# Kernel tuning notes

Hardware: AMD Instinct MI355X
Metric: run time of the kernel (lower is better)

The kernel has to match this reference:

```python
import jax, jax.numpy as jnp
import numpy as np

NC = 5  # num_clusters == unfold window size


def conv1x3(x, w, b):
    # x: (B, Cin, H, W); w: (Cout, Cin, 1, 3); padding (0,1) like torch Conv2d
    y = jax.lax.conv_general_dilated(
        x, w, window_strides=(1, 1), padding=((0, 0), (1, 1)),
        dimension_numbers=("NCHW", "OIHW", "NCHW"))
    return y + b[None, :, None, None]


def setup_inputs() -> dict:
    key = jax.random.key(0)
    ks = jax.random.split(key, 8)
    b, h, l, d = 8, 8, 1024, 64
    dm = h * d  # d_model = 512
    f32 = jnp.float32
    s_conv1 = 1.0 / np.sqrt(dm * 3)
    s_conv2 = 1.0 / np.sqrt(NC * 3)
    s_lin = 1.0 / np.sqrt(NC)
    return {
        "Q": jax.random.normal(ks[0], (b, h, l, d), f32),
        "K": jax.random.normal(ks[1], (b, h, l, d), f32),
        "V": jax.random.normal(ks[2], (b, h, l, d), f32),
        "w_proj_k": jax.random.normal(ks[3], (NC, dm, 1, 3), f32) * s_conv1,
        "b_proj_k": jnp.zeros((NC,), f32),
        "w_proj_back": jax.random.normal(ks[4], (dm, NC, 1, 3), f32) * s_conv2,
        "b_proj_back": jnp.zeros((dm,), f32),
        "w_ck": jax.random.normal(ks[5], (NC, NC), f32) * s_lin,
        "b_ck": jnp.zeros((NC,), f32),
        "w_cq": jax.random.normal(ks[6], (NC, NC), f32) * s_lin,
        "b_cq": jnp.zeros((NC,), f32),
    }


def reference(Q, K, V, w_proj_k, b_proj_k, w_proj_back, b_proj_back,
              w_ck, b_ck, w_cq, b_cq):
    b, h, l, d = Q.shape
    u = NC  # unfolding window
    # --- padded unfold along batch dim: window i is K_padded[i:i+u] ---
    K_padded = jnp.concatenate(
        [jnp.zeros((u, h, l, d), Q.dtype), K[1:]], axis=0)  # (u+b-1, h, l, d)
    idx = jnp.arange(b)[:, None] + jnp.arange(u)[None, :]     # (b, u)
    Kw = K_padded[idx]                                        # (b, u, h, l, d)
    Kw = jnp.transpose(Kw, (0, 2, 3, 4, 1))                   # (b, h, l, d, u) == torch unfold layout
    K_unfold = Kw.reshape(b, h * d, l, u)                     # raw reshape, matches torch
    # --- project to clusters ---
    ckp = jax.nn.relu(conv1x3(K_unfold, w_proj_k, b_proj_k))  # (b, NC, l, u)
    ckp = jnp.transpose(ckp, (0, 2, 3, 1))                    # (b, l, u, NC)
    cluster_k = jax.nn.softmax(ckp @ w_ck.T + b_ck, axis=-1)
    cluster_q = jax.nn.softmax(ckp @ w_cq.T + b_cq, axis=-1)
    # --- distributional loss ---
    mu = jnp.mean(cluster_q, axis=-1)                         # (b, l, u)
    sigma = jax.nn.softplus(jnp.std(cluster_q, axis=-1, ddof=1))  # unbiased std like torch
    x = jnp.mean(cluster_k, axis=-1)
    log_prob = -0.5 * ((x - mu) / sigma) ** 2 - jnp.log(sigma) - 0.5 * jnp.log(2 * jnp.pi)
    # CrossEntropyLoss(mu, mu): class dim is axis=1 (l); soft-label targets = mu
    ce = -jnp.mean(jnp.sum(mu * jax.nn.log_softmax(mu, axis=1), axis=1))
    loss = -jnp.mean(log_prob) + ce
    # --- masked triangular cluster attention ---
    scores = jnp.einsum('blpc,bluc->blpu', cluster_q, cluster_k) / u  # (b, l, u, u)
    mask = jnp.triu(jnp.ones((u, u), bool), k=1)
    scores = jnp.where(mask, -1e9, scores)
    attn = jax.nn.softmax(scores, axis=-1)
    cluster_q2 = jnp.einsum('blpu,bluc->blpc', attn, cluster_q)       # (b, l, u, NC)
    # --- project back & second attention ---
    cc = jax.nn.relu(conv1x3(jnp.transpose(cluster_q2, (0, 3, 1, 2)),
                             w_proj_back, b_proj_back))               # (b, h*d, l, u)
    cluster_center = cc.reshape(b, h, u, l, d)                        # raw reshape, matches torch
    scores_center = jnp.einsum('bhqd,bhckd->bhqk', Q, cluster_center) # sums over c and d
    attn2 = jax.nn.softmax(scores_center, axis=-1)
    context = jnp.einsum('bhqk,bhkd->bhqd', attn2, V)
    return (context, loss)
```

## Files before the change

kernel.cpp:

```cpp
#include <hip/hip_runtime.h>
#include <math.h>

#define L 1024
#define D 64
#define H 8
#define B 8

#define WS_G     0
#define WS_MU    107520
#define WS_Q2T   148480
#define WS_Q2T_BYTE   593920u
#define WS_DSC_BYTE   1740800u
#define WS_KHI_BYTE   1740816u
#define WS_KLO_BYTE   10129424u
#define WS_VTHI_BYTE  18518032u
#define WS_VTLO_BYTE  26906640u
#define WS_V_END      35295248u

typedef __attribute__((ext_vector_type(8))) short bf16x8;
typedef __attribute__((ext_vector_type(4))) float f32x4;

__device__ __forceinline__ ushort f2bf(float x) {
  unsigned b = __builtin_bit_cast(unsigned, x);
  return (ushort)((b + 0x7FFFu + ((b >> 16) & 1u)) >> 16);
}
__device__ __forceinline__ float bf2f(ushort u) {
  unsigned t = ((unsigned)u) << 16;
  return __builtin_bit_cast(float, t);
}

__global__ __launch_bounds__(256) void k_part(const float* __restrict__ K,
                                              const float* __restrict__ wpk,
                                              float* __restrict__ G) {
  const int tid = threadIdx.x, lane = tid & 63, wid = tid >> 6;
  const int lq = blockIdx.x;
  const int bip = blockIdx.y + 1;
  __shared__ float w_s[512 * 16];
  __shared__ float red[3][64][16];
  for (int i = tid; i < 512 * 16; i += 256) {
    int c = i >> 4, f = i & 15;
    w_s[i] = (f < 15) ? wpk[((f / 3) * 512 + c) * 3 + (f % 3)] : 0.f;
  }
  __syncthreads();
  float acc[15];
#pragma unroll
  for (int f = 0; f < 15; ++f) acc[f] = 0.f;
  const float* Kb = K + (size_t)bip * (H * L * D);
  const int c0 = wid * 128;
#pragma unroll 4
  for (int c = c0; c < c0 + 128; ++c) {
    float val = Kb[((c >> 6) * L + ((c & 63) << 4) + lq) * D + lane];
    const float4* wr = (const float4*)&w_s[c * 16];
    float4 w0 = wr[0], w1 = wr[1], w2 = wr[2], w3 = wr[3];
    acc[0] = fmaf(val, w0.x, acc[0]);  acc[1] = fmaf(val, w0.y, acc[1]);
    acc[2] = fmaf(val, w0.z, acc[2]);  acc[3] = fmaf(val, w0.w, acc[3]);
    acc[4] = fmaf(val, w1.x, acc[4]);  acc[5] = fmaf(val, w1.y, acc[5]);
    acc[6] = fmaf(val, w1.z, acc[6]);  acc[7] = fmaf(val, w1.w, acc[7]);
    acc[8] = fmaf(val, w2.x, acc[8]);  acc[9] = fmaf(val, w2.y, acc[9]);
    acc[10] = fmaf(val, w2.z, acc[10]); acc[11] = fmaf(val, w2.w, acc[11]);
    acc[12] = fmaf(val, w3.x, acc[12]); acc[13] = fmaf(val, w3.y, acc[13]);
    acc[14] = fmaf(val, w3.z, acc[14]);
  }
  if (wid) {
#pragma unroll
    for (int f = 0; f < 15; ++f) red[wid - 1][lane][f] = acc[f];
  }
  __syncthreads();
  if (wid == 0) {
#pragma unroll
    for (int f = 0; f < 15; ++f)
      acc[f] += red[0][lane][f] + red[1][lane][f] + red[2][lane][f];
    float* dst = G + ((size_t)blockIdx.y * 1024 + (lq << 6) + lane) * 15;
#pragma unroll
    for (int f = 0; f < 15; ++f) dst[f] = acc[f];
  }
}

__global__ __launch_bounds__(256) void k_chain(const float* __restrict__ G,
    const float* __restrict__ b_pk, const float* __restrict__ w_ck,
    const float* __restrict__ b_ck, const float* __restrict__ w_cq,
    const float* __restrict__ b_cq, float* __restrict__ mu_out,
    float* __restrict__ q2t, double* __restrict__ dsc) {
  int g = blockIdx.x * 256 + threadIdx.x;
  int bi = g >> 10, li = g & 1023;
  float ckp[5][5];
#pragma unroll
  for (int j = 0; j < 5; ++j) {
#pragma unroll
    for (int nc = 0; nc < 5; ++nc) {
      float s = b_pk[nc];
#pragma unroll
      for (int t = 0; t < 3; ++t) {
        int w = j + t - 1;
        int bip = bi + w - 4;
        if (w >= 0 && w < 5 && bip >= 1)
          s += G[(size_t)((bip - 1) * 1024 + li) * 15 + nc * 3 + t];
      }
      ckp[j][nc] = fmaxf(s, 0.f);
    }
  }
  float cq[5][5], ck[5][5];
  float lp_sum = 0.f;
#pragma unroll
  for (int j = 0; j < 5; ++j) {
    float vk[5], vq[5];
#pragma unroll
    for (int m = 0; m < 5; ++m) {
      float sk = b_ck[m], sq = b_cq[m];
#pragma unroll
      for (int n = 0; n < 5; ++n) {
        sk = fmaf(ckp[j][n], w_ck[m * 5 + n], sk);
        sq = fmaf(ckp[j][n], w_cq[m * 5 + n], sq);
      }
      vk[m] = sk; vq[m] = sq;
    }
    float mk = vk[0], mq = vq[0];
#pragma unroll
    for (int m = 1; m < 5; ++m) { mk = fmaxf(mk, vk[m]); mq = fmaxf(mq, vq[m]); }
    float sk = 0.f, sq = 0.f;
#pragma unroll
    for (int m = 0; m < 5; ++m) {
      vk[m] = expf(vk[m] - mk); sk += vk[m];
      vq[m] = expf(vq[m] - mq); sq += vq[m];
    }
    float rk = 1.f / sk, rq = 1.f / sq;
    float mu = 0.f, x = 0.f;
#pragma unroll
    for (int m = 0; m < 5; ++m) {
      ck[j][m] = vk[m] * rk; cq[j][m] = vq[m] * rq;
      mu += cq[j][m]; x += ck[j][m];
    }
    mu *= 0.2f; x *= 0.2f;
    float var = 0.f;
#pragma unroll
    for (int m = 0; m < 5; ++m) { float d0 = cq[j][m] - mu; var += d0 * d0; }
    var *= 0.25f;
    float sg = log1pf(expf(sqrtf(var)));
    float z = (x - mu) / sg;
    lp_sum += -0.5f * z * z - logf(sg) - 0.91893853320467274f;
    mu_out[(size_t)g * 5 + j] = mu;
  }
  float* q2p = q2t + (((size_t)bi * 35) << 10) + li;
#pragma unroll
  for (int pp = 0; pp < 5; ++pp) {
    float sc[5]; float mx = -3.0e38f;
    for (int u2 = 0; u2 <= pp; ++u2) {
      float d0 = 0.f;
#pragma unroll
      for (int c = 0; c < 5; ++c) d0 = fmaf(cq[pp][c], ck[u2][c], d0);
      sc[u2] = d0 * 0.2f;
      mx = fmaxf(mx, sc[u2]);
    }
    float den = 0.f;
    for (int u2 = 0; u2 <= pp; ++u2) { sc[u2] = expf(sc[u2] - mx); den += sc[u2]; }
    float rd = 1.f / den;
    float q2v[5] = {0.f, 0.f, 0.f, 0.f, 0.f};
    for (int u2 = 0; u2 <= pp; ++u2) {
      float a = sc[u2] * rd;
#pragma unroll
      for (int c = 0; c < 5; ++c) q2v[c] = fmaf(a, cq[u2][c], q2v[c]);
    }
#pragma unroll
    for (int c = 0; c < 5; ++c) q2p[(size_t)(((pp + 1) * 5 + c)) << 10] = q2v[c];
  }
  for (int off = 1; off < 64; off <<= 1) lp_sum += __shfl_xor(lp_sum, off, 64);
  __shared__ float wsum[4];
  int tid = threadIdx.x;
  if ((tid & 63) == 0) wsum[tid >> 6] = lp_sum;
  __syncthreads();
  if (tid == 0) atomicAdd(dsc, (double)(wsum[0] + wsum[1] + wsum[2] + wsum[3]));
}

__global__ __launch_bounds__(256) void k_ce(const float* __restrict__ mu,
                                            double* __restrict__ dsc) {
  int bi = blockIdx.x / 5, u = blockIdx.x % 5;
  int tid = threadIdx.x;
  const float* base = mu + (size_t)bi * L * 5 + u;
  float v[4];
#pragma unroll
  for (int k = 0; k < 4; ++k) v[k] = base[(tid + 256 * k) * 5];
  float mx = fmaxf(fmaxf(v[0], v[1]), fmaxf(v[2], v[3]));
  for (int off = 1; off < 64; off <<= 1) mx = fmaxf(mx, __shfl_xor(mx, off, 64));
  __shared__ float sh[4];
  if ((tid & 63) == 0) sh[tid >> 6] = mx;
  __syncthreads();
  mx = fmaxf(fmaxf(sh[0], sh[1]), fmaxf(sh[2], sh[3]));
  __syncthreads();
  float se = 0.f;
#pragma unroll
  for (int k = 0; k < 4; ++k) se += expf(v[k] - mx);
  for (int off = 1; off < 64; off <<= 1) se += __shfl_xor(se, off, 64);
  if ((tid & 63) == 0) sh[tid >> 6] = se;
  __syncthreads();
  float lse = mx + logf(sh[0] + sh[1] + sh[2] + sh[3]);
  __syncthreads();
  float part = 0.f;
#pragma unroll
  for (int k = 0; k < 4; ++k) part += v[k] * (v[k] - lse);
  for (int off = 1; off < 64; off <<= 1) part += __shfl_xor(part, off, 64);
  if ((tid & 63) == 0) sh[tid >> 6] = part;
  __syncthreads();
  if (tid == 0) atomicAdd(dsc + 1, (double)(sh[0] + sh[1] + sh[2] + sh[3]));
}

__global__ __launch_bounds__(256) void k_cback(const float* __restrict__ q2t,
    const float* __restrict__ wb, const float* __restrict__ bb,
    float* __restrict__ keff) {
  __shared__ float ls[1280];
  const int id = blockIdx.x;
  const int bi = id >> 11, cog = (id >> 4) & 127, lt = id & 15;
  const int tid = threadIdx.x, w = tid >> 6, lane = tid & 63;
  const int co = cog * 4 + w;
  const int li2 = (lt << 6) + lane;
  const float* xb = q2t + (((size_t)bi * 35) << 10) + li2;
  float xt[35];
#pragma unroll
  for (int k = 0; k < 35; ++k) xt[k] = xb[(size_t)k << 10];
  float wbl[15];
#pragma unroll
  for (int t = 0; t < 3; ++t)
#pragma unroll
    for (int c = 0; c < 5; ++c) wbl[t * 5 + c] = wb[co * 15 + c * 3 + t];
  const float bias = bb[co];
#pragma unroll
  for (int j = 0; j < 5; ++j) {
    float s = bias;
#pragma unroll
    for (int i = 0; i < 15; ++i) s = fmaf(xt[j * 5 + i], wbl[i], s);
    ls[w * 320 + lane * 5 + j] = fmaxf(s, 0.f);
  }
  __syncthreads();
  const int base_lo = (cog * 4) * 5120 + (lt << 6) * 5;
#pragma unroll
  for (int k = 0; k < 5; ++k) {
    int e = tid + (k << 8);
    float val = ls[e];
    int we = (int)((unsigned)e / 320u);
    int off = e - we * 320;
    int flat = base_lo + we * 5120 + off;
    int q = flat >> 16;
    int hh = (q * 205) >> 10;
    int idx = (((bi << 3) + hh) << 16) + (flat & 65535);
    atomicAdd(&keff[idx], val);
  }
}

__global__ __launch_bounds__(256) void k_kfold(const float* __restrict__ keff,
    ushort* __restrict__ Khi_g, ushort* __restrict__ Klo_g) {
  int g = blockIdx.x * 256 + threadIdx.x;
  float sum = keff[g];
  int li = (g >> 6) & 1023, dd = g & 63;
  int bh = g >> 16;
  int kt = li >> 6, key = li & 63, c = dd >> 2, e = dd & 3;
  int idx = ((bh * 16 + kt) << 12) + (key << 6) + ((c ^ (key & 15)) << 2) + e;
  ushort hb = f2bf(sum);
  Khi_g[idx] = hb;
  Klo_g[idx] = f2bf(sum - bf2f(hb));
}

__global__ __launch_bounds__(256) void k_vprep(const float* __restrict__ V,
    ushort* __restrict__ Vthi_g, ushort* __restrict__ Vtlo_g) {
  __shared__ float t[64][65];
  const int tile = blockIdx.x;
  const float* Vb = V + ((size_t)tile << 12);
  const int tid = threadIdx.x;
  {
    int key = tid >> 2, c0 = (tid & 3) << 4;
#pragma unroll
    for (int i = 0; i < 4; ++i) {
      float4 v = *(const float4*)(Vb + key * 64 + c0 + 4 * i);
      t[key][c0 + 4 * i + 0] = v.x; t[key][c0 + 4 * i + 1] = v.y;
      t[key][c0 + 4 * i + 2] = v.z; t[key][c0 + 4 * i + 3] = v.w;
    }
  }
  __syncthreads();
  int d = tid >> 2, q4 = tid & 3;
#pragma unroll
  for (int q = 0; q < 4; ++q) {
    int kc = q4 * 4 + q;
    ushort hv[4], lv[4];
#pragma unroll
    for (int e = 0; e < 4; ++e) {
      float x = t[kc * 4 + e][d];
      ushort hb = f2bf(x);
      hv[e] = hb;
      lv[e] = f2bf(x - bf2f(hb));
    }
    int idx = (tile << 12) + (d << 6) + ((kc ^ (d & 15)) << 2);
    ushort4 h4; h4.x = hv[0]; h4.y = hv[1]; h4.z = hv[2]; h4.w = hv[3];
    ushort4 l4; l4.x = lv[0]; l4.y = lv[1]; l4.z = lv[2]; l4.w = lv[3];
    *(ushort4*)(&Vthi_g[idx]) = h4;
    *(ushort4*)(&Vtlo_g[idx]) = l4;
  }
}

template<bool VPREP>
__global__ __launch_bounds__(256) void k_attn(const float* __restrict__ Q,
    const ushort* __restrict__ Khi_g, const ushort* __restrict__ Klo_g,
    const ushort* __restrict__ Vthi_g, const ushort* __restrict__ Vtlo_g,
    const float* __restrict__ V, float* __restrict__ Out) {
  __shared__ ushort smem[2][16384];
  const int tid = threadIdx.x;
  const int lane = tid & 63;
  const int w = tid >> 6;
  const int lq = lane & 15;
  const int g = lane >> 4;
  const int id = blockIdx.x;
  const int bh = ((id & 7) << 3) + (id >> 6);
  const int qb = (id >> 3) & 7;
  const int q0 = qb << 7;
  const float* Qb = Q + ((size_t)bh * L + q0 + w * 32) * D;
  const float* Vb = V + (size_t)bh * L * D;
  const int tb = bh * 16;

  int cx0 = ((g) ^ lq) << 2, cx1 = ((g + 4) ^ lq) << 2;
  int cx2 = ((g + 8) ^ lq) << 2, cx3 = ((g + 12) ^ lq) << 2;

  bf16x8 qh[2][2], qlo[2][2];
#pragma unroll
  for (int qs = 0; qs < 2; ++qs) {
    const float* Qr = Qb + (qs * 16 + lq) * D;
#pragma unroll
    for (int ds = 0; ds < 2; ++ds) {
      float4 x0 = *(const float4*)(Qr + 4 * g + 32 * ds);
      float4 x1 = *(const float4*)(Qr + 4 * g + 16 + 32 * ds);
      float xs[8] = {x0.x, x0.y, x0.z, x0.w, x1.x, x1.y, x1.z, x1.w};
      bf16x8 h, l;
#pragma unroll
      for (int j = 0; j < 8; ++j) {
        ushort hb = f2bf(xs[j]);
        h[j] = (short)hb;
        l[j] = (short)f2bf(xs[j] - bf2f(hb));
      }
      qh[qs][ds] = h; qlo[qs][ds] = l;
    }
  }

  const ushort* warr;
  int wdst;
  if (VPREP) {
    warr = (w == 0) ? Khi_g : (w == 1) ? Klo_g : (w == 2) ? Vthi_g : Vtlo_g;
    wdst = w << 12;
  } else {
    warr = ((w < 2) ? Khi_g : Klo_g);
    wdst = ((w >> 1) << 12) + ((w & 1) << 11);
  }

#define STAGE(buf_, kt_) do {                                                  \
    const ushort* src_ = warr + ((size_t)(tb + (kt_)) << 12) +                 \
                         (VPREP ? 0 : ((w & 1) << 11)) + lane * 8;             \
    ushort* dst_ = &smem[buf_][wdst];                                          \
    _Pragma("unroll")                                                          \
    for (int r_ = 0; r_ < (VPREP ? 8 : 4); ++r_) {                             \
      __builtin_amdgcn_global_load_lds(                                        \
        (const __attribute__((address_space(1))) unsigned int*)(src_ + r_ * 512), \
        (__attribute__((address_space(3))) unsigned int*)(dst_ + r_ * 512 + lane * 8), \
        16, 0, 0);                                                             \
    }                                                                          \
  } while (0)

  float4 vreg[2][2];
  const int kp = tid & 31, dblk = tid >> 5;
#define VLOAD(kt_) do {                                                        \
    const float* Vb2_ = Vb + ((size_t)(kt_) << 12);                            \
    _Pragma("unroll")                                                          \
    for (int kk_ = 0; kk_ < 2; ++kk_)                                          \
      _Pragma("unroll")                                                        \
      for (int i_ = 0; i_ < 2; ++i_)                                           \
        vreg[kk_][i_] = *(const float4*)(Vb2_ + (2 * kp + kk_) * 64 + dblk * 8 + 4 * i_); \
  } while (0)
#define VWRITE(nb_) do {                                                       \
    ushort vh_[2][8], vl_[2][8];                                               \
    _Pragma("unroll")                                                          \
    for (int kk_ = 0; kk_ < 2; ++kk_)                                          \
      _Pragma("unroll")                                                        \
      for (int i_ = 0; i_ < 2; ++i_) {                                         \
        float xs_[4] = {vreg[kk_][i_].x, vreg[kk_][i_].y, vreg[kk_][i_].z, vreg[kk_][i_].w}; \
        _Pragma("unroll")                                                      \
        for (int e_ = 0; e_ < 4; ++e_) {                                       \
          ushort hb_ = f2bf(xs_[e_]);                                          \
          vh_[kk_][4 * i_ + e_] = hb_;                                         \
          vl_[kk_][4 * i_ + e_] = f2bf(xs_[e_] - bf2f(hb_));                   \
        }                                                                      \
      }                                                                        \
    _Pragma("unroll")                                                          \
    for (int dd_ = 0; dd_ < 8; ++dd_) {                                        \
      int d_ = dblk * 8 + dd_;                                                 \
      int idx_ = (d_ << 6) + (((kp >> 1) ^ (d_ & 15)) << 2) + ((kp & 1) << 1); \
      ushort2 ph_; ph_.x = vh_[0][dd_]; ph_.y = vh_[1][dd_];                   \
      ushort2 pl_; pl_.x = vl_[0][dd_]; pl_.y = vl_[1][dd_];                   \
      *(ushort2*)(&smem[nb_][8192 + idx_]) = ph_;                              \
      *(ushort2*)(&smem[nb_][12288 + idx_]) = pl_;                             \
    }                                                                          \
  } while (0)

  f32x4 O_[2][4];
  float m_[2], l_[2];
#pragma unroll
  for (int qs = 0; qs < 2; ++qs) {
    m_[qs] = -3.0e38f; l_[qs] = 0.f;
#pragma unroll
    for (int d2 = 0; d2 < 4; ++d2) O_[qs][d2] = (f32x4){0.f, 0.f, 0.f, 0.f};
  }

  STAGE(0, 0);
  if (!VPREP) { VLOAD(0); VWRITE(0); }
  __syncthreads();

  int cur = 0;
  for (int kt = 0; kt < 16; ++kt) {
    if (kt < 15) {
      STAGE(cur ^ 1, kt + 1);
      if (!VPREP) VLOAD(kt + 1);
    }

    const ushort* Kh = &smem[cur][0];
    const ushort* Kl = &smem[cur][4096];
    const ushort* Vh = &smem[cur][8192];
    const ushort* Vl = &smem[cur][12288];

    f32x4 S[4][2];
#pragma unroll
    for (int ks = 0; ks < 4; ++ks)
#pragma unroll
      for (int qs = 0; qs < 2; ++qs) S[ks][qs] = (f32x4){0.f, 0.f, 0.f, 0.f};
#pragma unroll
    for (int ds = 0; ds < 2; ++ds) {
      int ca = ds ? cx2 : cx0, cb = ds ? cx3 : cx1;
#pragma unroll
      for (int ksub = 0; ksub < 4; ++ksub) {
        int base = (ksub * 16 + lq) * 64;
        ushort4 a0 = *(const ushort4*)(Kh + base + ca);
        ushort4 a1 = *(const ushort4*)(Kh + base + cb);
        ushort4 b0 = *(const ushort4*)(Kl + base + ca);
        ushort4 b1 = *(const ushort4*)(Kl + base + cb);
        bf16x8 kh = {(short)a0.x, (short)a0.y, (short)a0.z, (short)a0.w,
                     (short)a1.x, (short)a1.y, (short)a1.z, (short)a1.w};
        bf16x8 kl = {(short)b0.x, (short)b0.y, (short)b0.z, (short)b0.w,
                     (short)b1.x, (short)b1.y, (short)b1.z, (short)b1.w};
#pragma unroll
        for (int qs = 0; qs < 2; ++qs) {
          S[ksub][qs] = __builtin_amdgcn_mfma_f32_16x16x32_bf16(kh, qh[qs][ds], S[ksub][qs], 0, 0, 0);
          S[ksub][qs] = __builtin_amdgcn_mfma_f32_16x16x32_bf16(kh, qlo[qs][ds], S[ksub][qs], 0, 0, 0);
          S[ksub][qs] = __builtin_amdgcn_mfma_f32_16x16x32_bf16(kl, qh[qs][ds], S[ksub][qs], 0, 0, 0);
        }
      }
    }

    bf16x8 pfh[2][2];
    float scl[2];
#pragma unroll
    for (int qs = 0; qs < 2; ++qs) {
      float tmax = -3.0e38f;
#pragma unroll
      for (int ks = 0; ks < 4; ++ks)
#pragma unroll
        for (int r = 0; r < 4; ++r) tmax = fmaxf(tmax, S[ks][qs][r]);
      tmax = fmaxf(tmax, __shfl_xor(tmax, 16, 64));
      tmax = fmaxf(tmax, __shfl_xor(tmax, 32, 64));
      float mn = fmaxf(m_[qs], tmax);
      scl[qs] = __expf(m_[qs] - mn);
      float p[4][4]; float rs = 0.f;
#pragma unroll
      for (int ks = 0; ks < 4; ++ks)
#pragma unroll
        for (int r = 0; r < 4; ++r) {
          float pv = __expf(S[ks][qs][r] - mn);
          p[ks][r] = pv; rs += pv;
        }
      rs += __shfl_xor(rs, 16, 64);
      rs += __shfl_xor(rs, 32, 64);
      l_[qs] = l_[qs] * scl[qs] + rs;
      m_[qs] = mn;
#pragma unroll
      for (int kst = 0; kst < 2; ++kst) {
        bf16x8 h;
#pragma unroll
        for (int jh = 0; jh < 2; ++jh)
#pragma unroll
          for (int j2 = 0; j2 < 4; ++j2)
            h[jh * 4 + j2] = (short)f2bf(p[jh + 2 * kst][j2]);
        pfh[qs][kst] = h;
      }
#pragma unroll
      for (int d2 = 0; d2 < 4; ++d2)
#pragma unroll
        for (int r = 0; r < 4; ++r) O_[qs][d2][r] *= scl[qs];
    }

#pragma unroll
    for (int kst = 0; kst < 2; ++kst) {
      int ca = kst ? cx2 : cx0, cb = kst ? cx3 : cx1;
#pragma unroll
      for (int d2 = 0; d2 < 4; ++d2) {
        int base = (d2 * 16 + lq) * 64;
        ushort4 a0 = *(const ushort4*)(Vh + base + ca);
        ushort4 a1 = *(const ushort4*)(Vh + base + cb);
        ushort4 b0 = *(const ushort4*)(Vl + base + ca);
        ushort4 b1 = *(const ushort4*)(Vl + base + cb);
        bf16x8 vh = {(short)a0.x, (short)a0.y, (short)a0.z, (short)a0.w,
                     (short)a1.x, (short)a1.y, (short)a1.z, (short)a1.w};
        bf16x8 vl = {(short)b0.x, (short)b0.y, (short)b0.z, (short)b0.w,
                     (short)b1.x, (short)b1.y, (short)b1.z, (short)b1.w};
#pragma unroll
        for (int qs = 0; qs < 2; ++qs) {
          O_[qs][d2] = __builtin_amdgcn_mfma_f32_16x16x32_bf16(vh, pfh[qs][kst], O_[qs][d2], 0, 0, 0);
          O_[qs][d2] = __builtin_amdgcn_mfma_f32_16x16x32_bf16(vl, pfh[qs][kst], O_[qs][d2], 0, 0, 0);
        }
      }
    }

    if (!VPREP && kt < 15) VWRITE(cur ^ 1);
    __syncthreads();
    cur ^= 1;
  }

  float* Ob = Out + ((size_t)bh * L + q0 + w * 32) * D;
#pragma unroll
  for (int qs = 0; qs < 2; ++qs) {
    float il = 1.f / l_[qs];
    int q = qs * 16 + lq;
#pragma unroll
    for (int d2 = 0; d2 < 4; ++d2) {
      float4 o4;
      o4.x = O_[qs][d2][0] * il; o4.y = O_[qs][d2][1] * il;
      o4.z = O_[qs][d2][2] * il; o4.w = O_[qs][d2][3] * il;
      *(float4*)(Ob + q * D + d2 * 16 + 4 * g) = o4;
    }
  }
#undef STAGE
#undef VLOAD
#undef VWRITE
}

__global__ void k_final(const double* __restrict__ dsc, float* __restrict__ out) {
  out[4194304] = (float)(-dsc[0] / 40960.0 - dsc[1] / 40.0);
}

extern "C" void kernel_launch(void* const* d_in, const int* in_sizes, int n_in,
                              void* d_out, int out_size, void* d_ws, size_t ws_size,
                              hipStream_t stream) {
  const float* Q   = (const float*)d_in[0];
  const float* K   = (const float*)d_in[1];
  const float* V   = (const float*)d_in[2];
  const float* wpk = (const float*)d_in[3];
  const float* bpk = (const float*)d_in[4];
  const float* wpb = (const float*)d_in[5];
  const float* bpb = (const float*)d_in[6];
  const float* wck = (const float*)d_in[7];
  const float* bck = (const float*)d_in[8];
  const float* wcq = (const float*)d_in[9];
  const float* bcq = (const float*)d_in[10];
  float* out = (float*)d_out;
  float* ws = (float*)d_ws;
  float* G    = ws + WS_G;
  float* mu   = ws + WS_MU;
  float* q2t  = ws + WS_Q2T;
  double* dsc = (double*)((char*)d_ws + WS_DSC_BYTE);
  ushort* Khi = (ushort*)((char*)d_ws + WS_KHI_BYTE);
  ushort* Klo = (ushort*)((char*)d_ws + WS_KLO_BYTE);
  ushort* Vthi = (ushort*)((char*)d_ws + WS_VTHI_BYTE);
  ushort* Vtlo = (ushort*)((char*)d_ws + WS_VTLO_BYTE);
  const bool vprep = (ws_size >= (size_t)WS_V_END);
  float* keff = out;

  hipMemsetAsync((char*)d_ws + WS_Q2T_BYTE, 0, (WS_DSC_BYTE - WS_Q2T_BYTE) + 16, stream);
  hipMemsetAsync(out, 0, (size_t)4194304 * 4, stream);
  if (vprep) k_vprep<<<1024, 256, 0, stream>>>(V, Vthi, Vtlo);
  k_part<<<dim3(16, 7), 256, 0, stream>>>(K, wpk, G);
  k_chain<<<32, 256, 0, stream>>>(G, bpk, wck, bck, wcq, bcq, mu, q2t, dsc);
  k_ce<<<40, 256, 0, stream>>>(mu, dsc);
  k_cback<<<16384, 256, 0, stream>>>(q2t, wpb, bpb, keff);
  k_kfold<<<16384, 256, 0, stream>>>(keff, Khi, Klo);
  if (vprep) {
    k_attn<true><<<512, 256, 0, stream>>>(Q, Khi, Klo, Vthi, Vtlo, V, out);
  } else {
    k_attn<false><<<512, 256, 0, stream>>>(Q, Khi, Klo, nullptr, nullptr, V, out);
  }
  k_final<<<1, 1, 0, stream>>>(dsc, out);
}
```

Before: 293.6 us.

## Fuse projection-back conv with K fold and drop atomic accumulation into output

Replaces the conv-back kernel, which scatters atomic adds into a zeroed output buffer, and the separate fold/split kernel with one gather-style kernel. Each thread computes the eight summed cluster-center values for its key/dim positions directly from q2t staged in shared memory, then writes the hi/lo bf16 split in the swizzled layout. This removes the 16 MB memset, 4M float atomics and one full read pass of the intermediate. The cost is heavier per-thread index math with divisions and an extra shared-memory staging loop per cluster slice.

```diff
diff --git a/kernel.cpp b/kernel.cpp
--- a/kernel.cpp
+++ b/kernel.cpp
@@ -203,59 +203,75 @@
   if (tid == 0) atomicAdd(dsc + 1, (double)(sh[0] + sh[1] + sh[2] + sh[3]));
 }
 
-__global__ __launch_bounds__(256) void k_cback(const float* __restrict__ q2t,
+__global__ __launch_bounds__(256) void k_kback(const float* __restrict__ q2t,
     const float* __restrict__ wb, const float* __restrict__ bb,
-    float* __restrict__ keff) {
-  __shared__ float ls[1280];
+    ushort* __restrict__ Khi_g, ushort* __restrict__ Klo_g) {
+  __shared__ float lq[35 * 449];
+  __shared__ float w_s2[32];
+  __shared__ float bias2[2];
   const int id = blockIdx.x;
-  const int bi = id >> 11, cog = (id >> 4) & 127, lt = id & 15;
-  const int tid = threadIdx.x, w = tid >> 6, lane = tid & 63;
-  const int co = cog * 4 + w;
-  const int li2 = (lt << 6) + lane;
-  const float* xb = q2t + (((size_t)bi * 35) << 10) + li2;
-  float xt[35];
-#pragma unroll
-  for (int k = 0; k < 35; ++k) xt[k] = xb[(size_t)k << 10];
-  float wbl[15];
-#pragma unroll
-  for (int t = 0; t < 3; ++t)
-#pragma unroll
-    for (int c = 0; c < 5; ++c) wbl[t * 5 + c] = wb[co * 15 + c * 3 + t];
-  const float bias = bb[co];
-#pragma unroll
-  for (int j = 0; j < 5; ++j) {
-    float s = bias;
-#pragma unroll
-    for (int i = 0; i < 15; ++i) s = fmaf(xt[j * 5 + i], wbl[i], s);
-    ls[w * 320 + lane * 5 + j] = fmaxf(s, 0.f);
-  }
-  __syncthreads();
-  const int base_lo = (cog * 4) * 5120 + (lt << 6) * 5;
-#pragma unroll
-  for (int k = 0; k < 5; ++k) {
-    int e = tid + (k << 8);
-    float val = ls[e];
-    int we = (int)((unsigned)e / 320u);
-    int off = e - we * 320;
-    int flat = base_lo + we * 5120 + off;
-    int q = flat >> 16;
-    int hh = (q * 205) >> 10;
-    int idx = (((bi << 3) + hh) << 16) + (flat & 65535);
-    atomicAdd(&keff[idx], val);
-  }
-}
-
-__global__ __launch_bounds__(256) void k_kfold(const float* __restrict__ keff,
-    ushort* __restrict__ Khi_g, ushort* __restrict__ Klo_g) {
-  int g = blockIdx.x * 256 + threadIdx.x;
-  float sum = keff[g];
-  int li = (g >> 6) & 1023, dd = g & 63;
-  int bh = g >> 16;
-  int kt = li >> 6, key = li & 63, c = dd >> 2, e = dd & 3;
-  int idx = ((bh * 16 + kt) << 12) + (key << 6) + ((c ^ (key & 15)) << 2) + e;
-  ushort hb = f2bf(sum);
-  Khi_g[idx] = hb;
-  Klo_g[idx] = f2bf(sum - bf2f(hb));
+  const int bi = id >> 8, hh = (id >> 5) & 7, xt = id & 31;
+  const int x0 = xt << 11;
+  const int tid = threadIdx.x;
+  const float* q2b = q2t + (((size_t)bi * 35) << 10);
+  float acc[8];
+#pragma unroll
+  for (int e = 0; e < 8; ++e) acc[e] = 0.f;
+
+  for (int cc = 0; cc < 5; ++cc) {
+    const int base = (5 * hh + cc) * 65536 + x0;
+    const unsigned d5base = (unsigned)base / 5u;
+    const int l0 = d5base & 1023;
+    const int co0 = d5base >> 10;
+    __syncthreads();
+    for (int k = tid; k < 35 * 416; k += 256) {
+      int t = (int)((unsigned)k / 416u);
+      int i = k - t * 416;
+      lq[t * 449 + i] = q2b[(t << 10) + ((l0 + i) & 1023)];
+    }
+    if (tid < 32) {
+      int cr = tid >> 4, f = tid & 15;
+      int coe = min(co0 + cr, 511);
+      if (f < 15) w_s2[cr * 16 + f] = wb[coe * 15 + (f % 5) * 3 + (f / 5)];
+      else bias2[cr] = bb[coe];
+    }
+    __syncthreads();
+#pragma unroll
+    for (int e = 0; e < 8; ++e) {
+      unsigned p = (unsigned)(base + (tid << 3) + e);
+      unsigned d5 = p / 5u;
+      int j = (int)(p - 5u * d5);
+      int iidx = (int)(d5 - d5base);
+      int cr = (int)(d5 >> 10) - co0;
+      float s = bias2[cr];
+      const float* row = &lq[j * 2245 + iidx];
+      const float* wr = &w_s2[cr * 16];
+#pragma unroll
+      for (int ii = 0; ii < 15; ++ii) s = fmaf(row[ii * 449], wr[ii], s);
+      acc[e] += fmaxf(s, 0.f);
+    }
+  }
+
+  const int x = x0 + (tid << 3);
+  const int li = x >> 6, dd = x & 63;
+  const int kt = li >> 6, key = li & 63, c0i = dd >> 2;
+  const int bimg = (((bi * 8 + hh) * 16 + kt) << 12) + (key << 6);
+  const int ca = ((c0i ^ (key & 15)) << 2);
+  const int cb = (((c0i + 1) ^ (key & 15)) << 2);
+  ushort4 h0, h1, lo0, lo1;
+  ushort hb;
+  hb = f2bf(acc[0]); h0.x = hb; lo0.x = f2bf(acc[0] - bf2f(hb));
+  hb = f2bf(acc[1]); h0.y = hb; lo0.y = f2bf(acc[1] - bf2f(hb));
+  hb = f2bf(acc[2]); h0.z = hb; lo0.z = f2bf(acc[2] - bf2f(hb));
+  hb = f2bf(acc[3]); h0.w = hb; lo0.w = f2bf(acc[3] - bf2f(hb));
+  hb = f2bf(acc[4]); h1.x = hb; lo1.x = f2bf(acc[4] - bf2f(hb));
+  hb = f2bf(acc[5]); h1.y = hb; lo1.y = f2bf(acc[5] - bf2f(hb));
+  hb = f2bf(acc[6]); h1.z = hb; lo1.z = f2bf(acc[6] - bf2f(hb));
+  hb = f2bf(acc[7]); h1.w = hb; lo1.w = f2bf(acc[7] - bf2f(hb));
+  *(ushort4*)(&Khi_g[bimg + ca]) = h0;
+  *(ushort4*)(&Khi_g[bimg + cb]) = h1;
+  *(ushort4*)(&Klo_g[bimg + ca]) = lo0;
+  *(ushort4*)(&Klo_g[bimg + cb]) = lo1;
 }
 
 __global__ __launch_bounds__(256) void k_vprep(const float* __restrict__ V,
@@ -562,16 +578,13 @@
   ushort* Vthi = (ushort*)((char*)d_ws + WS_VTHI_BYTE);
   ushort* Vtlo = (ushort*)((char*)d_ws + WS_VTLO_BYTE);
   const bool vprep = (ws_size >= (size_t)WS_V_END);
-  float* keff = out;
 
   hipMemsetAsync((char*)d_ws + WS_Q2T_BYTE, 0, (WS_DSC_BYTE - WS_Q2T_BYTE) + 16, stream);
-  hipMemsetAsync(out, 0, (size_t)4194304 * 4, stream);
   if (vprep) k_vprep<<<1024, 256, 0, stream>>>(V, Vthi, Vtlo);
   k_part<<<dim3(16, 7), 256, 0, stream>>>(K, wpk, G);
   k_chain<<<32, 256, 0, stream>>>(G, bpk, wck, bck, wcq, bcq, mu, q2t, dsc);
   k_ce<<<40, 256, 0, stream>>>(mu, dsc);
-  k_cback<<<16384, 256, 0, stream>>>(q2t, wpb, bpb, keff);
-  k_kfold<<<16384, 256, 0, stream>>>(keff, Khi, Klo);
+  k_kback<<<2048, 256, 0, stream>>>(q2t, wpb, bpb, Khi, Klo);
   if (vprep) {
     k_attn<true><<<512, 256, 0, stream>>>(Q, Khi, Klo, Vthi, Vtlo, V, out);
   } else {
```

Result: slower. 415.7 us (+41.6%).
